# Performance work log

Hardware: AMD Instinct MI355X
Metric: run time of the kernel (lower is better)

## Reference

```python
import jax, jax.numpy as jnp
import numpy as np
from jax import lax

B, K, Z, C, H, W = 32, 7, 64, 3, 64, 64
G = H + 6  # decoder grid for 'small' variant
ITERS = 3
SCALE = Z ** -0.5
EPS = 1e-8


def _pe(h, w):
    # matches SlotAttention.create_positional_embedding: shape [w, h, 4]
    ww = jnp.linspace(0.0, 1.0, w)
    hh = jnp.linspace(0.0, 1.0, h)
    a = jnp.broadcast_to((1.0 - ww)[:, None], (w, h))  # dist_right
    b = jnp.broadcast_to(ww[:, None], (w, h))          # dist_left
    c = jnp.broadcast_to(hh[None, :], (w, h))          # dist_top
    d = jnp.broadcast_to((1.0 - hh)[None, :], (w, h))  # dist_bottom
    return jnp.stack([a, b, c, d], -1)


def _ln(x, g, b):
    m = x.mean(-1, keepdims=True)
    v = ((x - m) ** 2).mean(-1, keepdims=True)
    return (x - m) * lax.rsqrt(v + 1e-5) * g + b


def _conv(x, w, b, p):
    y = lax.conv_general_dilated(x, w, (1, 1), [(p, p), (p, p)],
                                 dimension_numbers=('NCHW', 'OIHW', 'NCHW'))
    return y + b[None, :, None, None]


def setup_inputs() -> dict:
    key = jax.random.key(0)
    ks = iter(jax.random.split(key, 64))
    nrm = lambda shape, s=0.05: jax.random.normal(next(ks), shape, jnp.float32) * s
    d = {}
    d['inputs'] = jax.random.normal(next(ks), (B, C, H, W), jnp.float32)
    d['noise'] = jax.random.normal(next(ks), (B * K, Z), jnp.float32)
    d['enc_pos_w'] = nrm((4, 64)); d['enc_pos_b'] = jnp.zeros(64, jnp.float32)
    d['ec1_w'] = nrm((64, 3, 5, 5)); d['ec1_b'] = jnp.zeros(64, jnp.float32)
    d['ec2_w'] = nrm((64, 64, 5, 5)); d['ec2_b'] = jnp.zeros(64, jnp.float32)
    d['ec3_w'] = nrm((64, 64, 5, 5)); d['ec3_b'] = jnp.zeros(64, jnp.float32)
    d['ec4_w'] = nrm((64, 64, 5, 5)); d['ec4_b'] = jnp.zeros(64, jnp.float32)
    d['ln1_g'] = jnp.ones(64, jnp.float32); d['ln1_b'] = jnp.zeros(64, jnp.float32)
    d['fc1_w'] = nrm((64, 64)); d['fc1_b'] = jnp.zeros(64, jnp.float32)
    d['fc2_w'] = nrm((64, 64)); d['fc2_b'] = jnp.zeros(64, jnp.float32)
    d['lns_g'] = jnp.ones(Z, jnp.float32); d['lns_b'] = jnp.zeros(Z, jnp.float32)
    d['lnf_g'] = jnp.ones(Z, jnp.float32); d['lnf_b'] = jnp.zeros(Z, jnp.float32)
    d['q_w'] = nrm((Z, Z)); d['k_w'] = nrm((64, Z)); d['v_w'] = nrm((64, Z))
    d['mlp1_w'] = nrm((Z, 128)); d['mlp1_b'] = jnp.zeros(128, jnp.float32)
    d['mlp2_w'] = nrm((128, Z)); d['mlp2_b'] = jnp.zeros(Z, jnp.float32)
    d['gru_wih'] = nrm((3 * Z, Z)); d['gru_whh'] = nrm((3 * Z, Z))
    d['gru_bih'] = jnp.zeros(3 * Z, jnp.float32); d['gru_bhh'] = jnp.zeros(3 * Z, jnp.float32)
    d['init_slots'] = jnp.concatenate([jnp.zeros((1, Z), jnp.float32), jnp.ones((1, Z), jnp.float32)], 1)
    d['dec_pos_w'] = nrm((4, Z)); d['dec_pos_b'] = jnp.zeros(Z, jnp.float32)
    d['dc1_w'] = nrm((32, Z, 5, 5)); d['dc1_b'] = jnp.zeros(32, jnp.float32)
    d['dc2_w'] = nrm((32, 32, 5, 5)); d['dc2_b'] = jnp.zeros(32, jnp.float32)
    d['dc3_w'] = nrm((32, 32, 5, 5)); d['dc3_b'] = jnp.zeros(32, jnp.float32)
    d['dc4_w'] = nrm((4, 32, 3, 3)); d['dc4_b'] = jnp.zeros(4, jnp.float32)
    return d


def _forward(inputs, noise, enc_pos_w, enc_pos_b, ec1_w, ec1_b, ec2_w, ec2_b,
             ec3_w, ec3_b, ec4_w, ec4_b, ln1_g, ln1_b, fc1_w, fc1_b, fc2_w, fc2_b,
             lns_g, lns_b, lnf_g, lnf_b, q_w, k_w, v_w, mlp1_w, mlp1_b, mlp2_w,
             mlp2_b, gru_wih, gru_whh, gru_bih, gru_bhh, init_slots, dec_pos_w,
             dec_pos_b, dc1_w, dc1_b, dc2_w, dc2_b, dc3_w, dc3_b, dc4_w, dc4_b):
    # ---- encoder ----
    h = jax.nn.relu(_conv(inputs, ec1_w, ec1_b, 2))
    h = jax.nn.relu(_conv(h, ec2_w, ec2_b, 2))
    h = jax.nn.relu(_conv(h, ec3_w, ec3_b, 2))
    h = jax.nn.relu(_conv(h, ec4_w, ec4_b, 2))
    h = h.transpose(0, 2, 3, 1)                        # [B,H,W,64]
    pe = _pe(H, W) @ enc_pos_w + enc_pos_b             # [W,H,64] (H==W)
    h = h + pe[None]
    feat = h.reshape(B, H * W, 64)
    feat = _ln(feat, ln1_g, ln1_b)
    feat = jax.nn.relu(feat @ fc1_w + fc1_b) @ fc2_w + fc2_b
    k = feat @ k_w                                     # [B,N,Z]
    v = feat @ v_w
    # ---- slot init: Normal(loc, softplus(sp)).rsample() ----
    loc, sp = jnp.split(init_slots, 2, axis=1)
    slots = (loc + jax.nn.softplus(sp) * noise).reshape(B, K, Z)
    # ---- iterative slot attention ----
    for _ in range(ITERS):
        prev = slots
        q = (_ln(prev, lns_g, lns_b) @ q_w) * SCALE
        dots = jnp.einsum('bid,bjd->bij', q, k)        # [B,K,N]
        attn = jax.nn.softmax(dots, axis=1) + EPS      # normalize over slots
        attn = attn / attn.sum(-1, keepdims=True)      # renormalize over keys
        updates = jnp.einsum('bjd,bij->bid', v, attn)  # [B,K,Z]
        # GRU cell (single step), torch gate order r,z,n
        gi = updates.reshape(-1, Z) @ gru_wih.T + gru_bih
        gh = prev.reshape(-1, Z) @ gru_whh.T + gru_bhh
        ir, iz, inn = jnp.split(gi, 3, -1)
        hr, hz, hn = jnp.split(gh, 3, -1)
        r = jax.nn.sigmoid(ir + hr)
        zg = jax.nn.sigmoid(iz + hz)
        n = jnp.tanh(inn + r * hn)
        slots = ((1.0 - zg) * n + zg * prev.reshape(-1, Z)).reshape(B, K, Z)
        slots = slots + (jax.nn.relu(_ln(slots, lnf_g, lnf_b) @ mlp1_w + mlp1_b) @ mlp2_w + mlp2_b)
    # ---- spatial-broadcast decoder ('small') ----
    flat = slots.reshape(B * K, Z)
    zb = jnp.broadcast_to(flat[:, :, None, None], (B * K, Z, G, G))
    pe_d = (_pe(G, G) @ dec_pos_w + dec_pos_b).transpose(2, 0, 1)  # [Z,G,G]
    zb = zb + pe_d[None]
    o = jax.nn.relu(_conv(zb, dc1_w, dc1_b, 1))        # 70->68
    o = jax.nn.relu(_conv(o, dc2_w, dc2_b, 1))         # 68->66
    o = jax.nn.relu(_conv(o, dc3_w, dc3_b, 1))         # 66->64
    o = _conv(o, dc4_w, dc4_b, 1)                      # 64->64, 4ch
    x_loc = jax.nn.sigmoid(o[:, :3]).reshape(B, K, C, H, W)
    mask_logits = o[:, 3].reshape(B, K, 1, H, W)
    mask_logp = jax.nn.log_softmax(mask_logits, axis=1)
    x_orig = (inputs + 1.0) / 2.0
    recon = (x_loc * jnp.exp(mask_logp)).sum(1)
    mse = ((x_orig - recon) ** 2).sum() / B
    return mse, x_loc, mask_logp, slots


def reference(inputs, noise, enc_pos_w, enc_pos_b, ec1_w, ec1_b, ec2_w, ec2_b,
              ec3_w, ec3_b, ec4_w, ec4_b, ln1_g, ln1_b, fc1_w, fc1_b, fc2_w, fc2_b,
              lns_g, lns_b, lnf_g, lnf_b, q_w, k_w, v_w, mlp1_w, mlp1_b, mlp2_w,
              mlp2_b, gru_wih, gru_whh, gru_bih, gru_bhh, init_slots, dec_pos_w,
              dec_pos_b, dc1_w, dc1_b, dc2_w, dc2_b, dc3_w, dc3_b, dc4_w, dc4_b):
    return _forward(inputs, noise, enc_pos_w, enc_pos_b, ec1_w, ec1_b, ec2_w, ec2_b,
                    ec3_w, ec3_b, ec4_w, ec4_b, ln1_g, ln1_b, fc1_w, fc1_b, fc2_w, fc2_b,
                    lns_g, lns_b, lnf_g, lnf_b, q_w, k_w, v_w, mlp1_w, mlp1_b, mlp2_w,
                    mlp2_b, gru_wih, gru_whh, gru_bih, gru_bhh, init_slots, dec_pos_w,
                    dec_pos_b, dc1_w, dc1_b, dc2_w, dc2_b, dc3_w, dc3_b, dc4_w, dc4_b)
```

## Files before the change

kernel.cpp:

```cpp
#include <hip/hip_runtime.h>
#include <math.h>

typedef short bf16x8 __attribute__((ext_vector_type(8)));
typedef float f32x4 __attribute__((ext_vector_type(4)));

#define WS_B0   0u
#define WS_B1   4194304u
#define WS_K    8388608u
#define WS_V    16777216u
#define WS_ATTN 25165824u
#define WS_PART 26083328u
#define WS_ZP   26312704u
#define WS_SLOT 26327040u
#define WS_ROW  26341376u
#define SCALE_ 0.125f

#define OFF_PEB   0u
#define OFF_WCLS  160000u
#define OFF_S     180000u
#define OFF_ZB    250000u

__device__ __forceinline__ float wave_sum(float v) {
#pragma unroll
    for (int m = 32; m >= 1; m >>= 1) v += __shfl_xor(v, m, 64);
    return v;
}
__device__ __forceinline__ unsigned short f2bf(float f) {
    unsigned u = __float_as_uint(f);
    u = u + 0x7fffu + ((u >> 16) & 1u);
    return (unsigned short)(u >> 16);
}
__device__ __forceinline__ float bf2f(unsigned short h) {
    return __uint_as_float(((unsigned)h) << 16);
}
__device__ __forceinline__ void gl_lds16(const void* src, void* lds_base) {
    __builtin_amdgcn_global_load_lds(
        (const __attribute__((address_space(1))) unsigned int*)src,
        (__attribute__((address_space(3))) unsigned int*)lds_base,
        16, 0, 0);
}

__global__ __launch_bounds__(256) void pack_weights(
    const float* __restrict__ w, unsigned short* __restrict__ wp,
    int CIN, int COUT_STORE, int KS, int NT, int total)
{
    int t = blockIdx.x * 256 + threadIdx.x;
    if (t >= total) return;
    int lane = t & 63;
    int nt = (t >> 6) % NT;
    int ch = t / (64 * NT);
    int CPT = CIN / 32;
    int cic = ch % CPT;
    int tap = ch / CPT;
    int ky = tap / KS, kx = tap % KS;
    int co = nt * 16 + (lane & 15);
    int k0 = cic * 32 + (lane >> 4) * 8;
    unsigned short v[8];
#pragma unroll
    for (int j = 0; j < 8; ++j) {
        int ci = k0 + j;
        float f = (co < COUT_STORE) ? w[((size_t)(co * CIN + ci) * KS + ky) * KS + kx] : 0.f;
        v[j] = f2bf(f);
    }
    *(uint4*)(wp + (size_t)t * 8) = *(uint4*)v;
}

__global__ __launch_bounds__(256) void pack_weights3(
    const float* __restrict__ w0, const float* __restrict__ w1,
    const float* __restrict__ w2, unsigned short* __restrict__ wp,
    float* __restrict__ zpage)
{
    if (blockIdx.x == 0 && threadIdx.x < 64) zpage[threadIdx.x] = 0.f;
    int t = blockIdx.x * 256 + threadIdx.x;
    if (t >= 38400) return;
    int which = t / 12800;
    int tt = t % 12800;
    const float* w = (which == 0) ? w0 : ((which == 1) ? w1 : w2);
    unsigned short* dst = wp + (size_t)which * 102400;
    int lane = tt & 63;
    int nt = (tt >> 6) & 3;
    int ch = tt >> 8;
    int cic = ch & 1;
    int tap = ch >> 1;
    int ky = tap / 5, kx = tap % 5;
    int co = nt * 16 + (lane & 15);
    int k0 = cic * 32 + (lane >> 4) * 8;
    unsigned short v[8];
#pragma unroll
    for (int j = 0; j < 8; ++j) {
        int ci = k0 + j;
        v[j] = f2bf(w[((size_t)(co * 64 + ci) * 5 + ky) * 5 + kx]);
    }
    *(uint4*)(dst + (size_t)tt * 8) = *(uint4*)v;
}

__global__ __launch_bounds__(256) void pack_fc4(
    const float* __restrict__ w0, const float* __restrict__ w1,
    const float* __restrict__ w2, const float* __restrict__ w3,
    unsigned short* __restrict__ wp)
{
    int t = blockIdx.x * 256 + threadIdx.x;
    if (t >= 2048) return;
    int which = t / 512;
    int tt = t % 512;
    const float* w = (which == 0) ? w0 : ((which == 1) ? w1 : ((which == 2) ? w2 : w3));
    unsigned short* dst = wp + (size_t)which * 4096;
    int lane = tt & 63;
    int nt = (tt >> 6) & 3;
    int ck = tt >> 8;
    int n = nt * 16 + (lane & 15);
    int k0 = ck * 32 + (lane >> 4) * 8;
    unsigned short v[8];
#pragma unroll
    for (int j = 0; j < 8; ++j) v[j] = f2bf(w[(size_t)(k0 + j) * 64 + n]);
    *(uint4*)(dst + (size_t)tt * 8) = *(uint4*)v;
}

template<int CIN, int NTT, int NTU, int KS, int PAD, int NSTORE, int RELU, int OUTF32>
__global__ __launch_bounds__(256) void conv_mfma(
    const unsigned short* __restrict__ in, const unsigned short* __restrict__ wpack,
    const float* __restrict__ bias, void* __restrict__ outv,
    const unsigned short* __restrict__ zpage,
    int Hin, int Win, int Hout, int Wout, int tilesX, int tilesY)
{
    constexpr int TS = 16, TH = TS + KS - 1;
    constexpr int CPT = CIN / 32;
    constexpr int G8 = CIN / 8;
    constexpr int CS = NTT / NTU;
    constexpr int TOTCH = TH * TH * G8;
    constexpr int TOTCH_PAD = (TOTCH + 63) & ~63;
    __shared__ __align__(16) unsigned short tile[TOTCH_PAD * 8];
    const int tpb = tilesX * tilesY;
    const int blk = blockIdx.x;
    const int n = blk / (tpb * CS);
    const int rem = blk % (tpb * CS);
    const int t = rem / CS;
    const int cog = rem % CS;
    const int ntb = cog * NTU;
    const int ty0 = (t / tilesX) * TS, tx0 = (t % tilesX) * TS;
    const int tid = threadIdx.x;
    const int wv = tid >> 6, lane = tid & 63;

    const unsigned short* inb = in + (size_t)n * Hin * Win * CIN;
    for (int cb = wv * 64; cb < TOTCH; cb += 256) {
        const int idx = cb + lane;
        const int r = idx / (TH * G8);
        const int p = idx % (TH * G8);
        const int c = p / G8;
        const int chunk = p % G8;
        const int g = (chunk - c) & (G8 - 1);
        const int iy = ty0 - PAD + r, ix = tx0 - PAD + c;
        const bool ok = (idx < TOTCH) && ((unsigned)iy < (unsigned)Hin) && ((unsigned)ix < (unsigned)Win);
        const unsigned short* src = ok ? (inb + ((size_t)iy * Win + ix) * CIN + g * 8) : zpage;
        gl_lds16(src, tile + (size_t)cb * 8);
    }
    __syncthreads();

    const int q = lane >> 4, m = lane & 15;
    const int row0 = wv * 4;
    f32x4 acc[4][NTU];
#pragma unroll
    for (int mt = 0; mt < 4; ++mt)
#pragma unroll
        for (int nt = 0; nt < NTU; ++nt) acc[mt][nt] = (f32x4){0.f, 0.f, 0.f, 0.f};

#pragma unroll
    for (int cic = 0; cic < CPT; ++cic) {
#pragma unroll
        for (int kx = 0; kx < KS; ++kx) {
            bf16x8 B[KS][NTU];
#pragma unroll
            for (int ky = 0; ky < KS; ++ky)
#pragma unroll
                for (int nt = 0; nt < NTU; ++nt)
                    B[ky][nt] = *(const bf16x8*)(wpack +
                        ((size_t)(((ky * KS + kx) * CPT + cic) * NTT + ntb + nt) * 64 + lane) * 8);
            const int cbase = m + kx;
            const int slot = (cic * 32 + q * 8 + cbase * 8) % CIN;
#pragma unroll
            for (int ir = 0; ir < KS + 3; ++ir) {
                bf16x8 afr = *(const bf16x8*)&tile[((row0 + ir) * TH + cbase) * CIN + slot];
#pragma unroll
                for (int ky = 0; ky < KS; ++ky) {
                    const int mt = ir - ky;
                    if (mt < 0 || mt > 3) continue;
#pragma unroll
                    for (int nt = 0; nt < NTU; ++nt)
                        acc[mt][nt] = __builtin_amdgcn_mfma_f32_16x16x32_bf16(afr, B[ky][nt], acc[mt][nt], 0, 0, 0);
                }
            }
        }
    }

#pragma unroll
    for (int nt = 0; nt < NTU; ++nt) {
        const int co = (ntb + nt) * 16 + m;
        const float bv = (co < NSTORE) ? bias[co] : 0.f;
#pragma unroll
        for (int mt = 0; mt < 4; ++mt) {
            const int oy = ty0 + wv * 4 + mt;
#pragma unroll
            for (int j = 0; j < 4; ++j) {
                const int ox = tx0 + q * 4 + j;
                if (oy < Hout && ox < Wout && co < NSTORE) {
                    float v = acc[mt][nt][j] + bv;
                    if (RELU) v = fmaxf(v, 0.f);
                    size_t o = (((size_t)n * Hout + oy) * Wout + ox) * NSTORE + co;
                    if (OUTF32) ((float*)outv)[o] = v;
                    else ((unsigned short*)outv)[o] = f2bf(v);
                }
            }
        }
    }
}

__global__ __launch_bounds__(256) void pe_synth(
    const float* __restrict__ dpw, const float* __restrict__ dpb,
    unsigned short* __restrict__ peb, float* __restrict__ zbias)
{
    const int tid = threadIdx.x;
    if (blockIdx.x == 0 && tid < 32) zbias[tid] = 0.f;
    const int pix = blockIdx.x * 256 + tid;
    if (pix >= 4900) return;
    const int iy = pix / 70, ix = pix % 70;
    const float fy = iy * (1.f / 69.f), fx = ix * (1.f / 69.f);
    unsigned short v[64];
#pragma unroll
    for (int ci = 0; ci < 64; ++ci) {
        float p = (1.f - fy) * dpw[ci] + fy * dpw[64 + ci]
                + fx * dpw[128 + ci] + (1.f - fx) * dpw[192 + ci] + dpb[ci];
        v[ci] = f2bf(p);
    }
    uint4* ob = (uint4*)(peb + (size_t)pix * 64);
#pragma unroll
    for (int i = 0; i < 8; ++i) ob[i] = ((uint4*)v)[i];
}

__global__ __launch_bounds__(256) void wcls_build(
    const float* __restrict__ w, float* __restrict__ wcls)
{
    int idx = blockIdx.x * 256 + threadIdx.x;
    if (idx >= 9 * 32 * 64) return;
    int cls = idx / (32 * 64);
    int co = (idx / 64) % 32;
    int ci = idx % 64;
    int rc = cls / 3, cc = cls % 3;
    int ky0 = (rc == 0) ? 1 : 0, ky1 = (rc == 2) ? 3 : 4;
    int kx0 = (cc == 0) ? 1 : 0, kx1 = (cc == 2) ? 3 : 4;
    float s = 0.f;
    const float* wb = w + (size_t)(co * 64 + ci) * 25;
    for (int ky = ky0; ky <= ky1; ++ky)
        for (int kx = kx0; kx <= kx1; ++kx)
            s += wb[ky * 5 + kx];
    wcls[idx] = s;
}

__global__ __launch_bounds__(256) void slot_s(
    const float* __restrict__ slots, const float* __restrict__ wcls,
    float* __restrict__ S)
{
    int idx = blockIdx.x * 256 + threadIdx.x;
    if (idx >= 224 * 9 * 32) return;
    int n = idx / (9 * 32);
    int cls = (idx / 32) % 9;
    int co = idx % 32;
    const float* sl = slots + n * 64;
    const float* wc = wcls + (size_t)(cls * 32 + co) * 64;
    float s = 0.f;
#pragma unroll
    for (int ci = 0; ci < 64; ++ci) s = fmaf(sl[ci], wc[ci], s);
    S[idx] = s;
}

__global__ __launch_bounds__(256) void dc1_assemble(
    const float* __restrict__ P, const float* __restrict__ S,
    const float* __restrict__ bias, int n0,
    unsigned short* __restrict__ out)
{
    const int gid = blockIdx.x * 256 + threadIdx.x;
    const int nl = gid / 4624;
    const int pix = gid % 4624;
    const int oy = pix / 68, ox = pix % 68;
    const int rc = (oy == 0) ? 0 : ((oy == 67) ? 2 : 1);
    const int cc = (ox == 0) ? 0 : ((ox == 67) ? 2 : 1);
    const float* Sp = S + ((size_t)(n0 + nl) * 9 + (rc * 3 + cc)) * 32;
    const float* Pp = P + (size_t)pix * 32;
    unsigned short v[32];
#pragma unroll
    for (int co = 0; co < 32; ++co)
        v[co] = f2bf(fmaxf(bias[co] + Pp[co] + Sp[co], 0.f));
    uint4* ob = (uint4*)(out + ((size_t)nl * 4624 + pix) * 32);
#pragma unroll
    for (int i = 0; i < 4; ++i) ob[i] = ((uint4*)v)[i];
}

__global__ __launch_bounds__(256) void conv_ec1(
    const float* __restrict__ in, const float* __restrict__ wts,
    const float* __restrict__ bias, unsigned short* __restrict__ out)
{
    __shared__ float tile[3][20][21];
    const int blk = blockIdx.x;
    const int n = blk >> 6;
    const int sub = blk & 63;
    const int t = sub >> 2;
    const int cog = sub & 3;
    const int ty0 = (t >> 2) * 16, tx0 = (t & 3) * 16;
    const int tid = threadIdx.x;
    for (int idx = tid; idx < 1200; idx += 256) {
        int ci = idx / 400, rc = idx % 400;
        int r = rc / 20, c = rc % 20;
        int gy = ty0 + r - 2, gx = tx0 + c - 2;
        float v = 0.f;
        if (gy >= 0 && gy < 64 && gx >= 0 && gx < 64)
            v = in[((size_t)n * 3 + ci) * 4096 + gy * 64 + gx];
        tile[ci][r][c] = v;
    }
    __syncthreads();
    const int lx = tid & 15, ly = tid >> 4;
    float acc[16];
#pragma unroll
    for (int co = 0; co < 16; ++co) acc[co] = bias[cog * 16 + co];
    for (int ci = 0; ci < 3; ++ci) {
        float val[25];
#pragma unroll
        for (int ky = 0; ky < 5; ++ky)
#pragma unroll
            for (int kx = 0; kx < 5; ++kx) val[ky * 5 + kx] = tile[ci][ly + ky][lx + kx];
#pragma unroll
        for (int co = 0; co < 16; ++co) {
            const float* wc = wts + (size_t)((cog * 16 + co) * 3 + ci) * 25;
            float a = acc[co];
#pragma unroll
            for (int tt = 0; tt < 25; ++tt) a = fmaf(val[tt], wc[tt], a);
            acc[co] = a;
        }
    }
    unsigned short tmp[16];
#pragma unroll
    for (int co = 0; co < 16; ++co) tmp[co] = f2bf(fmaxf(acc[co], 0.f));
    uint4* ob = (uint4*)(out + (((size_t)n * 64 + ty0 + ly) * 64 + tx0 + lx) * 64 + cog * 16);
    ob[0] = ((uint4*)tmp)[0];
    ob[1] = ((uint4*)tmp)[1];
}

__global__ __launch_bounds__(256) void encoder_tail_mfma(
    const unsigned short* __restrict__ h4,
    const float* __restrict__ epw, const float* __restrict__ epb,
    const float* __restrict__ ln1g, const float* __restrict__ ln1b,
    const unsigned short* __restrict__ pfc1, const float* __restrict__ fc1b,
    const unsigned short* __restrict__ pfc2, const float* __restrict__ fc2b,
    const unsigned short* __restrict__ pkw, const unsigned short* __restrict__ pvw,
    unsigned short* __restrict__ kout, unsigned short* __restrict__ vout)
{
    __shared__ __align__(16) unsigned short X[64][72];
    const int b = blockIdx.x >> 6;
    const int y = blockIdx.x & 63;
    const int tid = threadIdx.x;

    {
        const int p = tid >> 2, sub = tid & 3;
        const unsigned short* hp = h4 + ((((size_t)b * 64 + y) * 64 + p) * 64) + sub * 16;
        unsigned short raw[16];
        *(uint4*)(raw)     = *(const uint4*)hp;
        *(uint4*)(raw + 8) = *(const uint4*)(hp + 8);
        const float fy = y * (1.f / 63.f), fx = p * (1.f / 63.f);
        float f[16];
        float s1 = 0.f, s2 = 0.f;
#pragma unroll
        for (int j = 0; j < 16; ++j) {
            int ch = sub * 16 + j;
            float pe = (1.f - fy) * epw[ch] + fy * epw[64 + ch]
                     + fx * epw[128 + ch] + (1.f - fx) * epw[192 + ch] + epb[ch];
            float v = bf2f(raw[j]) + pe;
            f[j] = v;
            s1 += v;
            s2 += v * v;
        }
        s1 += __shfl_xor(s1, 1, 64); s1 += __shfl_xor(s1, 2, 64);
        s2 += __shfl_xor(s2, 1, 64); s2 += __shfl_xor(s2, 2, 64);
        const float m = s1 * (1.f / 64.f);
        const float var = s2 * (1.f / 64.f) - m * m;
        const float inv = rsqrtf(var + 1e-5f);
        unsigned short xb[16];
#pragma unroll
        for (int j = 0; j < 16; ++j) {
            int ch = sub * 16 + j;
            xb[j] = f2bf((f[j] - m) * inv * ln1g[ch] + ln1b[ch]);
        }
        *(uint4*)&X[p][sub * 16]     = ((uint4*)xb)[0];
        *(uint4*)&X[p][sub * 16 + 8] = ((uint4*)xb)[1];
    }
    __syncthreads();

    const int w = tid >> 6, lane = tid & 63;
    const int q = lane >> 4, m_ = lane & 15;
    const int row0 = w * 16;

    {
        f32x4 a1[4];
#pragma unroll
        for (int nt = 0; nt < 4; ++nt) a1[nt] = (f32x4){0.f, 0.f, 0.f, 0.f};
#pragma unroll
        for (int ck = 0; ck < 2; ++ck) {
            bf16x8 afr = *(const bf16x8*)&X[row0 + m_][ck * 32 + q * 8];
#pragma unroll
            for (int nt = 0; nt < 4; ++nt) {
                bf16x8 bfr = *(const bf16x8*)(pfc1 + ((size_t)((ck * 4 + nt) * 64 + lane)) * 8);
                a1[nt] = __builtin_amdgcn_mfma_f32_16x16x32_bf16(afr, bfr, a1[nt], 0, 0, 0);
            }
        }
        __syncthreads();
#pragma unroll
        for (int nt = 0; nt < 4; ++nt) {
            const float bb = fc1b[nt * 16 + m_];
#pragma unroll
            for (int reg = 0; reg < 4; ++reg)
                X[row0 + q * 4 + reg][nt * 16 + m_] = f2bf(fmaxf(a1[nt][reg] + bb, 0.f));
        }
    }
    __syncthreads();

    {
        f32x4 a2[4];
#pragma unroll
        for (int nt = 0; nt < 4; ++nt) a2[nt] = (f32x4){0.f, 0.f, 0.f, 0.f};
#pragma unroll
        for (int ck = 0; ck < 2; ++ck) {
            bf16x8 afr = *(const bf16x8*)&X[row0 + m_][ck * 32 + q * 8];
#pragma unroll
            for (int nt = 0; nt < 4; ++nt) {
                bf16x8 bfr = *(const bf16x8*)(pfc2 + ((size_t)((ck * 4 + nt) * 64 + lane)) * 8);
                a2[nt] = __builtin_amdgcn_mfma_f32_16x16x32_bf16(afr, bfr, a2[nt], 0, 0, 0);
            }
        }
        __syncthreads();
#pragma unroll
        for (int nt = 0; nt < 4; ++nt) {
            const float bb = fc2b[nt * 16 + m_];
#pragma unroll
            for (int reg = 0; reg < 4; ++reg)
                X[row0 + q * 4 + reg][nt * 16 + m_] = f2bf(a2[nt][reg] + bb);
        }
    }
    __syncthreads();

    {
        f32x4 ak[4], av[4];
#pragma unroll
        for (int nt = 0; nt < 4; ++nt) {
            ak[nt] = (f32x4){0.f, 0.f, 0.f, 0.f};
            av[nt] = (f32x4){0.f, 0.f, 0.f, 0.f};
        }
#pragma unroll
        for (int ck = 0; ck < 2; ++ck) {
            bf16x8 afr = *(const bf16x8*)&X[row0 + m_][ck * 32 + q * 8];
#pragma unroll
            for (int nt = 0; nt < 4; ++nt) {
                bf16x8 bk = *(const bf16x8*)(pkw + ((size_t)((ck * 4 + nt) * 64 + lane)) * 8);
                bf16x8 bv = *(const bf16x8*)(pvw + ((size_t)((ck * 4 + nt) * 64 + lane)) * 8);
                ak[nt] = __builtin_amdgcn_mfma_f32_16x16x32_bf16(afr, bk, ak[nt], 0, 0, 0);
                av[nt] = __builtin_amdgcn_mfma_f32_16x16x32_bf16(afr, bv, av[nt], 0, 0, 0);
            }
        }
        const size_t base = ((size_t)b * 4096) + y * 64 + row0;
#pragma unroll
        for (int nt = 0; nt < 4; ++nt) {
            const int ch = nt * 16 + m_;
#pragma unroll
            for (int reg = 0; reg < 4; ++reg) {
                const size_t o = (base + q * 4 + reg) * 64 + ch;
                kout[o] = f2bf(ak[nt][reg]);
                vout[o] = f2bf(av[nt][reg]);
            }
        }
    }
}

__global__ __launch_bounds__(256) void slot_init(
    const float* __restrict__ noise, const float* __restrict__ init_slots,
    float* __restrict__ slots, float* __restrict__ rowsum)
{
    int i = blockIdx.x * 256 + threadIdx.x;
    if (i < 224) rowsum[i] = 0.f;
    if (i < 224 * 64) {
        int z = i & 63;
        float spl = log1pf(expf(init_slots[64 + z]));
        slots[i] = init_slots[z] + spl * noise[i];
    }
}

__global__ __launch_bounds__(256) void attn_fused(
    const unsigned short* __restrict__ kbuf, const unsigned short* __restrict__ vbuf,
    const float* __restrict__ slots,
    const float* __restrict__ lnsg, const float* __restrict__ lnsb,
    const float* __restrict__ qw,
    float* __restrict__ part, float* __restrict__ rowsum)
{
    __shared__ float qs[7][64];
    __shared__ float ash[256][7];
    __shared__ float red7[7][4];
    __shared__ float redv[4][7][64];
    const int b = blockIdx.x >> 4;
    const int js = blockIdx.x & 15;
    const int j0 = js * 256;
    const int tid = threadIdx.x;
    const int lane = tid & 63, wv = tid >> 6;

    for (int i = wv; i < 7; i += 4) {
        float s = slots[(b * 7 + i) * 64 + lane];
        float m = wave_sum(s) * (1.f / 64.f);
        float d = s - m;
        float var = wave_sum(d * d) * (1.f / 64.f);
        float x = d * rsqrtf(var + 1e-5f) * lnsg[lane] + lnsb[lane];
        float qv = 0.f;
        for (int c = 0; c < 64; ++c) qv = fmaf(__shfl(x, c, 64), qw[c * 64 + lane], qv);
        qs[i][lane] = qv * SCALE_;
    }
    __syncthreads();

    {
        const int j = j0 + tid;
        float kr[64];
        const unsigned short* kp = kbuf + (((size_t)b * 4096) + j) * 64;
#pragma unroll
        for (int d8 = 0; d8 < 8; ++d8) {
            uint4 kv = ((const uint4*)kp)[d8];
            const unsigned short* h = (const unsigned short*)&kv;
#pragma unroll
            for (int z = 0; z < 8; ++z) kr[d8 * 8 + z] = bf2f(h[z]);
        }
        float dots[7];
#pragma unroll
        for (int i = 0; i < 7; ++i) {
            float a = 0.f;
#pragma unroll
            for (int d = 0; d < 64; ++d) a = fmaf(kr[d], qs[i][d], a);
            dots[i] = a;
        }
        float mx = dots[0];
#pragma unroll
        for (int i = 1; i < 7; ++i) mx = fmaxf(mx, dots[i]);
        float sum = 0.f;
#pragma unroll
        for (int i = 0; i < 7; ++i) { dots[i] = expf(dots[i] - mx); sum += dots[i]; }
        const float inv = 1.f / sum;
#pragma unroll
        for (int i = 0; i < 7; ++i) {
            float a = dots[i] * inv + 1e-8f;
            dots[i] = a;
            ash[tid][i] = a;
        }
#pragma unroll
        for (int i = 0; i < 7; ++i) {
            float s = wave_sum(dots[i]);
            if (lane == 0) red7[i][wv] = s;
        }
    }
    __syncthreads();
    if (tid < 7)
        atomicAdd(&rowsum[b * 7 + tid], red7[tid][0] + red7[tid][1] + red7[tid][2] + red7[tid][3]);

    {
        const int d = lane, jc = wv;
        float acc[7];
#pragma unroll
        for (int i = 0; i < 7; ++i) acc[i] = 0.f;
        for (int jl = jc; jl < 256; jl += 4) {
            float av = bf2f(vbuf[(((size_t)b * 4096) + j0 + jl) * 64 + d]);
#pragma unroll
            for (int i = 0; i < 7; ++i)
                acc[i] = fmaf(ash[jl][i], av, acc[i]);
        }
#pragma unroll
        for (int i = 0; i < 7; ++i) redv[jc][i][d] = acc[i];
    }
    __syncthreads();
    if (tid < 7 * 64) {
        int i = tid / 64, dd = tid % 64;
        float s = redv[0][i][dd] + redv[1][i][dd] + redv[2][i][dd] + redv[3][i][dd];
        part[((((size_t)b * 16) + js) * 7 + i) * 64 + dd] = s;
    }
}

__global__ __launch_bounds__(64) void gru_mlp(
    float* __restrict__ slots, const float* __restrict__ part,
    float* __restrict__ rowsum,
    const float* __restrict__ wih, const float* __restrict__ whh,
    const float* __restrict__ bih, const float* __restrict__ bhh,
    const float* __restrict__ lnfg, const float* __restrict__ lnfb,
    const float* __restrict__ m1w, const float* __restrict__ m1b,
    const float* __restrict__ m2w, const float* __restrict__ m2b)
{
    const int n = blockIdx.x;
    const int b = n / 7, i = n % 7;
    const int l = threadIdx.x;
    float upd = 0.f;
    for (int js = 0; js < 16; ++js)
        upd += part[((((size_t)b * 16) + js) * 7 + i) * 64 + l];
    upd /= rowsum[n];
    if (l == 0) rowsum[n] = 0.f;
    const float prev = slots[n * 64 + l];
    float gi0 = bih[l], gi1 = bih[64 + l], gi2 = bih[128 + l];
    float gh0 = bhh[l], gh1 = bhh[64 + l], gh2 = bhh[128 + l];
    for (int c = 0; c < 64; ++c) {
        float u = __shfl(upd, c, 64), p = __shfl(prev, c, 64);
        gi0 = fmaf(u, wih[l * 64 + c], gi0);
        gi1 = fmaf(u, wih[(64 + l) * 64 + c], gi1);
        gi2 = fmaf(u, wih[(128 + l) * 64 + c], gi2);
        gh0 = fmaf(p, whh[l * 64 + c], gh0);
        gh1 = fmaf(p, whh[(64 + l) * 64 + c], gh1);
        gh2 = fmaf(p, whh[(128 + l) * 64 + c], gh2);
    }
    float r  = 1.f / (1.f + expf(-(gi0 + gh0)));
    float zg = 1.f / (1.f + expf(-(gi1 + gh1)));
    float nn = tanhf(gi2 + r * gh2);
    float s = (1.f - zg) * nn + zg * prev;
    float m = wave_sum(s) * (1.f / 64.f);
    float d = s - m;
    float var = wave_sum(d * d) * (1.f / 64.f);
    float x = d * rsqrtf(var + 1e-5f) * lnfg[l] + lnfb[l];
    float h0 = m1b[l], h1 = m1b[64 + l];
    for (int c = 0; c < 64; ++c) {
        float xv = __shfl(x, c, 64);
        h0 = fmaf(xv, m1w[c * 128 + l], h0);
        h1 = fmaf(xv, m1w[c * 128 + 64 + l], h1);
    }
    h0 = fmaxf(h0, 0.f); h1 = fmaxf(h1, 0.f);
    float o = m2b[l];
    for (int c = 0; c < 64; ++c) {
        o = fmaf(__shfl(h0, c, 64), m2w[c * 64 + l], o);
        o = fmaf(__shfl(h1, c, 64), m2w[(64 + c) * 64 + l], o);
    }
    slots[n * 64 + l] = s + o;
}

__global__ __launch_bounds__(256) void finalize_k(
    const float* __restrict__ dc4out, const float* __restrict__ inputs,
    float* __restrict__ out)
{
    const int tid = threadIdx.x;
    const int gp = blockIdx.x * 256 + tid;
    const int b = gp >> 12, p = gp & 4095;
    float4 o4[7];
#pragma unroll
    for (int k = 0; k < 7; ++k)
        o4[k] = ((const float4*)dc4out)[(size_t)(b * 7 + k) * 4096 + p];
    float mx = o4[0].w;
#pragma unroll
    for (int k = 1; k < 7; ++k) mx = fmaxf(mx, o4[k].w);
    float s = 0.f;
#pragma unroll
    for (int k = 0; k < 7; ++k) s += expf(o4[k].w - mx);
    const float lse = mx + logf(s);
    float recon0 = 0.f, recon1 = 0.f, recon2 = 0.f;
    float* xl = out + 1;
    float* ml = out + 2752513;
#pragma unroll
    for (int k = 0; k < 7; ++k) {
        float lp = o4[k].w - lse;
        ml[((size_t)(b * 7 + k)) * 4096 + p] = lp;
        float w = expf(lp);
        float x0 = 1.f / (1.f + expf(-o4[k].x));
        float x1 = 1.f / (1.f + expf(-o4[k].y));
        float x2 = 1.f / (1.f + expf(-o4[k].z));
        xl[(((size_t)(b * 7 + k)) * 3 + 0) * 4096 + p] = x0;
        xl[(((size_t)(b * 7 + k)) * 3 + 1) * 4096 + p] = x1;
        xl[(((size_t)(b * 7 + k)) * 3 + 2) * 4096 + p] = x2;
        recon0 = fmaf(x0, w, recon0);
        recon1 = fmaf(x1, w, recon1);
        recon2 = fmaf(x2, w, recon2);
    }
    float err = 0.f;
    {
        float xo = (inputs[((size_t)b * 3 + 0) * 4096 + p] + 1.f) * 0.5f;
        float dd = xo - recon0; err += dd * dd;
        xo = (inputs[((size_t)b * 3 + 1) * 4096 + p] + 1.f) * 0.5f;
        dd = xo - recon1; err += dd * dd;
        xo = (inputs[((size_t)b * 3 + 2) * 4096 + p] + 1.f) * 0.5f;
        dd = xo - recon2; err += dd * dd;
    }
    float wsum = wave_sum(err);
    __shared__ float red[4];
    const int lane = tid & 63, wv = tid >> 6;
    if (lane == 0) red[wv] = wsum;
    __syncthreads();
    if (tid == 0) atomicAdd(out, (red[0] + red[1] + red[2] + red[3]) * (1.f / 32.f));
}

__global__ __launch_bounds__(256) void copy_slots(const float* __restrict__ slots,
                                                  float* __restrict__ out)
{
    int i = blockIdx.x * 256 + threadIdx.x;
    if (i == 0) out[0] = 0.f;
    if (i < 14336) out[3670017 + i] = slots[i];
}

extern "C" void kernel_launch(void* const* d_in, const int* in_sizes, int n_in,
                              void* d_out, int out_size, void* d_ws, size_t ws_size,
                              hipStream_t stream) {
    (void)in_sizes; (void)n_in; (void)out_size; (void)ws_size;
    const float* inputs = (const float*)d_in[0];
    const float* noise  = (const float*)d_in[1];
    const float* epw  = (const float*)d_in[2];
    const float* epb  = (const float*)d_in[3];
    const float* ec1w = (const float*)d_in[4];
    const float* ec1b = (const float*)d_in[5];
    const float* ec2w = (const float*)d_in[6];
    const float* ec2b = (const float*)d_in[7];
    const float* ec3w = (const float*)d_in[8];
    const float* ec3b = (const float*)d_in[9];
    const float* ec4w = (const float*)d_in[10];
    const float* ec4b = (const float*)d_in[11];
    const float* ln1g = (const float*)d_in[12];
    const float* ln1b = (const float*)d_in[13];
    const float* fc1w = (const float*)d_in[14];
    const float* fc1b = (const float*)d_in[15];
    const float* fc2w = (const float*)d_in[16];
    const float* fc2b = (const float*)d_in[17];
    const float* lnsg = (const float*)d_in[18];
    const float* lnsb = (const float*)d_in[19];
    const float* lnfg = (const float*)d_in[20];
    const float* lnfb = (const float*)d_in[21];
    const float* qw   = (const float*)d_in[22];
    const float* kw   = (const float*)d_in[23];
    const float* vw   = (const float*)d_in[24];
    const float* m1w  = (const float*)d_in[25];
    const float* m1b  = (const float*)d_in[26];
    const float* m2w  = (const float*)d_in[27];
    const float* m2b  = (const float*)d_in[28];
    const float* wih  = (const float*)d_in[29];
    const float* whh  = (const float*)d_in[30];
    const float* bih  = (const float*)d_in[31];
    const float* bhh  = (const float*)d_in[32];
    const float* init_slots = (const float*)d_in[33];
    const float* dpw  = (const float*)d_in[34];
    const float* dpb  = (const float*)d_in[35];
    const float* dc1w = (const float*)d_in[36];
    const float* dc1b = (const float*)d_in[37];
    const float* dc2w = (const float*)d_in[38];
    const float* dc2b = (const float*)d_in[39];
    const float* dc3w = (const float*)d_in[40];
    const float* dc3b = (const float*)d_in[41];
    const float* dc4w = (const float*)d_in[42];
    const float* dc4b = (const float*)d_in[43];

    float* ws = (float*)d_ws;
    unsigned short* B0 = (unsigned short*)(ws + WS_B0);
    unsigned short* B1 = (unsigned short*)(ws + WS_B1);
    unsigned short* K = (unsigned short*)(ws + WS_K);
    unsigned short* V = (unsigned short*)(ws + WS_V);
    unsigned short* dping = (unsigned short*)(ws + WS_B0);
    unsigned short* dpong = (unsigned short*)(ws + WS_K);
    float* dc4out = ws + WS_V;
    unsigned short* PK = (unsigned short*)(ws + WS_V + 4194304u);
    unsigned short* p_ec2 = PK, *p_ec3 = PK + 102400, *p_ec4 = PK + 204800;
    unsigned short* p_dc1 = PK, *p_dc2 = PK + 51200, *p_dc3 = PK + 76800, *p_dc4 = PK + 102400;
    float* attn  = ws + WS_ATTN;
    unsigned short* PFC = (unsigned short*)attn;
    unsigned short* p_fc1 = PFC, *p_fc2 = PFC + 4096, *p_kw = PFC + 8192, *p_vw = PFC + 12288;
    unsigned short* peb = (unsigned short*)(attn + OFF_PEB);
    float* wclsb = attn + OFF_WCLS;
    float* Sbuf  = attn + OFF_S;
    float* zbias = attn + OFF_ZB;
    float* part  = ws + WS_PART;
    float* P     = ws + WS_PART;
    float* zpage = ws + WS_ZP;
    float* slots = ws + WS_SLOT;
    float* rowsum = ws + WS_ROW;
    float* out = (float*)d_out;
    const unsigned short* zp16 = (const unsigned short*)zpage;

    pack_weights3<<<150, 256, 0, stream>>>(ec2w, ec3w, ec4w, p_ec2, zpage);
    pack_fc4<<<8, 256, 0, stream>>>(fc1w, fc2w, kw, vw, p_fc1);

    conv_ec1<<<2048, 256, 0, stream>>>(inputs, ec1w, ec1b, B0);
    conv_mfma<64, 4, 4, 5, 2, 64, 1, 0><<<512, 256, 0, stream>>>(B0, p_ec2, ec2b, B1, zp16, 64, 64, 64, 64, 4, 4);
    conv_mfma<64, 4, 4, 5, 2, 64, 1, 0><<<512, 256, 0, stream>>>(B1, p_ec3, ec3b, B0, zp16, 64, 64, 64, 64, 4, 4);
    conv_mfma<64, 4, 4, 5, 2, 64, 1, 0><<<512, 256, 0, stream>>>(B0, p_ec4, ec4b, B1, zp16, 64, 64, 64, 64, 4, 4);
    encoder_tail_mfma<<<2048, 256, 0, stream>>>(B1, epw, epb, ln1g, ln1b,
                                                p_fc1, fc1b, p_fc2, fc2b, p_kw, p_vw, K, V);
    slot_init<<<56, 256, 0, stream>>>(noise, init_slots, slots, rowsum);

    for (int it = 0; it < 3; ++it) {
        attn_fused<<<512, 256, 0, stream>>>(K, V, slots, lnsg, lnsb, qw, part, rowsum);
        gru_mlp<<<224, 64, 0, stream>>>(slots, part, rowsum, wih, whh, bih, bhh,
                                        lnfg, lnfb, m1w, m1b, m2w, m2b);
    }

    pack_weights<<<25, 256, 0, stream>>>(dc1w, p_dc1, 64, 32, 5, 2, 6400);
    pack_weights<<<13, 256, 0, stream>>>(dc2w, p_dc2, 32, 32, 5, 2, 3200);
    pack_weights<<<13, 256, 0, stream>>>(dc3w, p_dc3, 32, 32, 5, 2, 3200);
    pack_weights<<<3, 256, 0, stream>>>(dc4w, p_dc4, 32, 4, 3, 1, 576);
    pe_synth<<<20, 256, 0, stream>>>(dpw, dpb, peb, zbias);
    conv_mfma<64, 2, 2, 5, 1, 32, 0, 1><<<25, 256, 0, stream>>>(peb, p_dc1, zbias, P, zp16, 70, 70, 68, 68, 5, 5);
    wcls_build<<<72, 256, 0, stream>>>(dc1w, wclsb);
    slot_s<<<252, 256, 0, stream>>>(slots, wclsb, Sbuf);

    for (int ch = 0; ch < 2; ++ch) {
        float* d4o = dc4out + (size_t)ch * 112 * 4 * 4096;
        dc1_assemble<<<2023, 256, 0, stream>>>(P, Sbuf, dc1b, ch * 112, dping);
        conv_mfma<32, 2, 2, 5, 1, 32, 1, 0><<<2800, 256, 0, stream>>>(dping, p_dc2, dc2b, dpong, zp16, 68, 68, 66, 66, 5, 5);
        conv_mfma<32, 2, 2, 5, 1, 32, 1, 0><<<1792, 256, 0, stream>>>(dpong, p_dc3, dc3b, dping, zp16, 66, 66, 64, 64, 4, 4);
        conv_mfma<32, 1, 1, 3, 1, 4, 0, 1><<<1792, 256, 0, stream>>>(dping, p_dc4, dc4b, d4o, zp16, 64, 64, 64, 64, 4, 4);
    }

    copy_slots<<<56, 256, 0, stream>>>(slots, out);
    finalize_k<<<512, 256, 0, stream>>>(dc4out, inputs, out);
}
```

Measured before the change: 741.0 us.

## Merge small prep kernels into fused launches and split encoder conv channels

```diff
diff --git a/kernel.cpp b/kernel.cpp
--- a/kernel.cpp
+++ b/kernel.cpp
@@ -16,7 +16,6 @@
 #define SCALE_ 0.125f
 
 #define OFF_PEB   0u
-#define OFF_WCLS  160000u
 #define OFF_S     180000u
 #define OFF_ZB    250000u
 
@@ -40,12 +39,10 @@
         16, 0, 0);
 }
 
-__global__ __launch_bounds__(256) void pack_weights(
+__device__ __forceinline__ void pack_one(
     const float* __restrict__ w, unsigned short* __restrict__ wp,
-    int CIN, int COUT_STORE, int KS, int NT, int total)
-{
-    int t = blockIdx.x * 256 + threadIdx.x;
-    if (t >= total) return;
+    int CIN, int COUT_STORE, int KS, int NT, int t)
+{
     int lane = t & 63;
     int nt = (t >> 6) % NT;
     int ch = t / (64 * NT);
@@ -65,55 +62,100 @@
     *(uint4*)(wp + (size_t)t * 8) = *(uint4*)v;
 }
 
-__global__ __launch_bounds__(256) void pack_weights3(
-    const float* __restrict__ w0, const float* __restrict__ w1,
-    const float* __restrict__ w2, unsigned short* __restrict__ wp,
-    float* __restrict__ zpage)
+__global__ __launch_bounds__(256) void pack_enc(
+    const float* __restrict__ ec2w, const float* __restrict__ ec3w,
+    const float* __restrict__ ec4w, unsigned short* __restrict__ wp,
+    const float* __restrict__ fc1w, const float* __restrict__ fc2w,
+    const float* __restrict__ kw, const float* __restrict__ vw,
+    unsigned short* __restrict__ pfc, float* __restrict__ zpage)
 {
     if (blockIdx.x == 0 && threadIdx.x < 64) zpage[threadIdx.x] = 0.f;
     int t = blockIdx.x * 256 + threadIdx.x;
-    if (t >= 38400) return;
-    int which = t / 12800;
-    int tt = t % 12800;
-    const float* w = (which == 0) ? w0 : ((which == 1) ? w1 : w2);
-    unsigned short* dst = wp + (size_t)which * 102400;
-    int lane = tt & 63;
-    int nt = (tt >> 6) & 3;
-    int ch = tt >> 8;
-    int cic = ch & 1;
-    int tap = ch >> 1;
-    int ky = tap / 5, kx = tap % 5;
-    int co = nt * 16 + (lane & 15);
-    int k0 = cic * 32 + (lane >> 4) * 8;
-    unsigned short v[8];
-#pragma unroll
-    for (int j = 0; j < 8; ++j) {
-        int ci = k0 + j;
-        v[j] = f2bf(w[((size_t)(co * 64 + ci) * 5 + ky) * 5 + kx]);
-    }
-    *(uint4*)(dst + (size_t)tt * 8) = *(uint4*)v;
-}
-
-__global__ __launch_bounds__(256) void pack_fc4(
-    const float* __restrict__ w0, const float* __restrict__ w1,
-    const float* __restrict__ w2, const float* __restrict__ w3,
-    unsigned short* __restrict__ wp)
+    if (t < 38400) {
+        int which = t / 12800;
+        int tt = t % 12800;
+        const float* w = (which == 0) ? ec2w : ((which == 1) ? ec3w : ec4w);
+        pack_one(w, wp + (size_t)which * 102400, 64, 64, 5, 4, tt);
+        return;
+    }
+    t -= 38400;
+    if (t < 2048) {
+        int which = t / 512;
+        int tt = t % 512;
+        const float* w = (which == 0) ? fc1w : ((which == 1) ? fc2w : ((which == 2) ? kw : vw));
+        unsigned short* dst = pfc + (size_t)which * 4096;
+        int lane = tt & 63;
+        int nt = (tt >> 6) & 3;
+        int ck = tt >> 8;
+        int n = nt * 16 + (lane & 15);
+        int k0 = ck * 32 + (lane >> 4) * 8;
+        unsigned short v[8];
+#pragma unroll
+        for (int j = 0; j < 8; ++j) v[j] = f2bf(w[(size_t)(k0 + j) * 64 + n]);
+        *(uint4*)(dst + (size_t)tt * 8) = *(uint4*)v;
+    }
+}
+
+__global__ __launch_bounds__(256) void dec_prep(
+    const float* __restrict__ dc1w, const float* __restrict__ dc2w,
+    const float* __restrict__ dc3w, const float* __restrict__ dc4w,
+    unsigned short* __restrict__ p_dc1, unsigned short* __restrict__ p_dc2,
+    unsigned short* __restrict__ p_dc3, unsigned short* __restrict__ p_dc4,
+    const float* __restrict__ dpw, const float* __restrict__ dpb,
+    unsigned short* __restrict__ peb, float* __restrict__ zbias,
+    const float* __restrict__ slots, float* __restrict__ S,
+    float* __restrict__ out)
 {
     int t = blockIdx.x * 256 + threadIdx.x;
-    if (t >= 2048) return;
-    int which = t / 512;
-    int tt = t % 512;
-    const float* w = (which == 0) ? w0 : ((which == 1) ? w1 : ((which == 2) ? w2 : w3));
-    unsigned short* dst = wp + (size_t)which * 4096;
-    int lane = tt & 63;
-    int nt = (tt >> 6) & 3;
-    int ck = tt >> 8;
-    int n = nt * 16 + (lane & 15);
-    int k0 = ck * 32 + (lane >> 4) * 8;
-    unsigned short v[8];
-#pragma unroll
-    for (int j = 0; j < 8; ++j) v[j] = f2bf(w[(size_t)(k0 + j) * 64 + n]);
-    *(uint4*)(dst + (size_t)tt * 8) = *(uint4*)v;
+    if (t < 6400) { pack_one(dc1w, p_dc1, 64, 32, 5, 2, t); return; }
+    t -= 6400;
+    if (t < 3200) { pack_one(dc2w, p_dc2, 32, 32, 5, 2, t); return; }
+    t -= 3200;
+    if (t < 3200) { pack_one(dc3w, p_dc3, 32, 32, 5, 2, t); return; }
+    t -= 3200;
+    if (t < 576)  { pack_one(dc4w, p_dc4, 32, 4, 3, 1, t); return; }
+    t -= 576;
+    if (t < 4900) {
+        const int iy = t / 70, ix = t % 70;
+        const float fy = iy * (1.f / 69.f), fx = ix * (1.f / 69.f);
+        unsigned short v[64];
+#pragma unroll
+        for (int ci = 0; ci < 64; ++ci) {
+            float p = (1.f - fy) * dpw[ci] + fy * dpw[64 + ci]
+                    + fx * dpw[128 + ci] + (1.f - fx) * dpw[192 + ci] + dpb[ci];
+            v[ci] = f2bf(p);
+        }
+        uint4* ob = (uint4*)(peb + (size_t)t * 64);
+#pragma unroll
+        for (int i = 0; i < 8; ++i) ob[i] = ((uint4*)v)[i];
+        return;
+    }
+    t -= 4900;
+    if (t < 224 * 9 * 32) {
+        int n = t / (9 * 32);
+        int cls = (t / 32) % 9;
+        int co = t % 32;
+        int rc = cls / 3, cc = cls % 3;
+        int ky0 = (rc == 0) ? 1 : 0, ky1 = (rc == 2) ? 3 : 4;
+        int kx0 = (cc == 0) ? 1 : 0, kx1 = (cc == 2) ? 3 : 4;
+        const float* sl = slots + n * 64;
+        float s = 0.f;
+        for (int ci = 0; ci < 64; ++ci) {
+            const float* wb = dc1w + (size_t)(co * 64 + ci) * 25;
+            float wsum = 0.f;
+            for (int ky = ky0; ky <= ky1; ++ky)
+                for (int kx = kx0; kx <= kx1; ++kx)
+                    wsum += wb[ky * 5 + kx];
+            s = fmaf(sl[ci], wsum, s);
+        }
+        S[t] = s;
+        return;
+    }
+    t -= 224 * 9 * 32;
+    if (t < 14336) { out[3670017 + t] = slots[t]; return; }
+    t -= 14336;
+    if (t < 32) zbias[t] = 0.f;
+    else if (t == 32) out[0] = 0.f;
 }
 
 template<int CIN, int NTT, int NTU, int KS, int PAD, int NSTORE, int RELU, int OUTF32>
@@ -212,64 +254,6 @@
             }
         }
     }
-}
-
-__global__ __launch_bounds__(256) void pe_synth(
-    const float* __restrict__ dpw, const float* __restrict__ dpb,
-    unsigned short* __restrict__ peb, float* __restrict__ zbias)
-{
-    const int tid = threadIdx.x;
-    if (blockIdx.x == 0 && tid < 32) zbias[tid] = 0.f;
-    const int pix = blockIdx.x * 256 + tid;
-    if (pix >= 4900) return;
-    const int iy = pix / 70, ix = pix % 70;
-    const float fy = iy * (1.f / 69.f), fx = ix * (1.f / 69.f);
-    unsigned short v[64];
-#pragma unroll
-    for (int ci = 0; ci < 64; ++ci) {
-        float p = (1.f - fy) * dpw[ci] + fy * dpw[64 + ci]
-                + fx * dpw[128 + ci] + (1.f - fx) * dpw[192 + ci] + dpb[ci];
-        v[ci] = f2bf(p);
-    }
-    uint4* ob = (uint4*)(peb + (size_t)pix * 64);
-#pragma unroll
-    for (int i = 0; i < 8; ++i) ob[i] = ((uint4*)v)[i];
-}
-
-__global__ __launch_bounds__(256) void wcls_build(
-    const float* __restrict__ w, float* __restrict__ wcls)
-{
-    int idx = blockIdx.x * 256 + threadIdx.x;
-    if (idx >= 9 * 32 * 64) return;
-    int cls = idx / (32 * 64);
-    int co = (idx / 64) % 32;
-    int ci = idx % 64;
-    int rc = cls / 3, cc = cls % 3;
-    int ky0 = (rc == 0) ? 1 : 0, ky1 = (rc == 2) ? 3 : 4;
-    int kx0 = (cc == 0) ? 1 : 0, kx1 = (cc == 2) ? 3 : 4;
-    float s = 0.f;
-    const float* wb = w + (size_t)(co * 64 + ci) * 25;
-    for (int ky = ky0; ky <= ky1; ++ky)
-        for (int kx = kx0; kx <= kx1; ++kx)
-            s += wb[ky * 5 + kx];
-    wcls[idx] = s;
-}
-
-__global__ __launch_bounds__(256) void slot_s(
-    const float* __restrict__ slots, const float* __restrict__ wcls,
-    float* __restrict__ S)
-{
-    int idx = blockIdx.x * 256 + threadIdx.x;
-    if (idx >= 224 * 9 * 32) return;
-    int n = idx / (9 * 32);
-    int cls = (idx / 32) % 9;
-    int co = idx % 32;
-    const float* sl = slots + n * 64;
-    const float* wc = wcls + (size_t)(cls * 32 + co) * 64;
-    float s = 0.f;
-#pragma unroll
-    for (int ci = 0; ci < 64; ++ci) s = fmaf(sl[ci], wc[ci], s);
-    S[idx] = s;
 }
 
 __global__ __launch_bounds__(256) void dc1_assemble(
@@ -685,14 +669,6 @@
     if (lane == 0) red[wv] = wsum;
     __syncthreads();
     if (tid == 0) atomicAdd(out, (red[0] + red[1] + red[2] + red[3]) * (1.f / 32.f));
-}
-
-__global__ __launch_bounds__(256) void copy_slots(const float* __restrict__ slots,
-                                                  float* __restrict__ out)
-{
-    int i = blockIdx.x * 256 + threadIdx.x;
-    if (i == 0) out[0] = 0.f;
-    if (i < 14336) out[3670017 + i] = slots[i];
 }
 
 extern "C" void kernel_launch(void* const* d_in, const int* in_sizes, int n_in,
@@ -757,9 +733,8 @@
     unsigned short* p_dc1 = PK, *p_dc2 = PK + 51200, *p_dc3 = PK + 76800, *p_dc4 = PK + 102400;
     float* attn  = ws + WS_ATTN;
     unsigned short* PFC = (unsigned short*)attn;
-    unsigned short* p_fc1 = PFC, *p_fc2 = PFC + 4096, *p_kw = PFC + 8192, *p_vw = PFC + 12288;
+    unsigned short* p_fc1 = PFC;
     unsigned short* peb = (unsigned short*)(attn + OFF_PEB);
-    float* wclsb = attn + OFF_WCLS;
     float* Sbuf  = attn + OFF_S;
     float* zbias = attn + OFF_ZB;
     float* part  = ws + WS_PART;
@@ -770,15 +745,16 @@
     float* out = (float*)d_out;
     const unsigned short* zp16 = (const unsigned short*)zpage;
 
-    pack_weights3<<<150, 256, 0, stream>>>(ec2w, ec3w, ec4w, p_ec2, zpage);
-    pack_fc4<<<8, 256, 0, stream>>>(fc1w, fc2w, kw, vw, p_fc1);
+    pack_enc<<<159, 256, 0, stream>>>(ec2w, ec3w, ec4w, p_ec2,
+                                      fc1w, fc2w, kw, vw, p_fc1, zpage);
 
     conv_ec1<<<2048, 256, 0, stream>>>(inputs, ec1w, ec1b, B0);
-    conv_mfma<64, 4, 4, 5, 2, 64, 1, 0><<<512, 256, 0, stream>>>(B0, p_ec2, ec2b, B1, zp16, 64, 64, 64, 64, 4, 4);
-    conv_mfma<64, 4, 4, 5, 2, 64, 1, 0><<<512, 256, 0, stream>>>(B1, p_ec3, ec3b, B0, zp16, 64, 64, 64, 64, 4, 4);
-    conv_mfma<64, 4, 4, 5, 2, 64, 1, 0><<<512, 256, 0, stream>>>(B0, p_ec4, ec4b, B1, zp16, 64, 64, 64, 64, 4, 4);
+    conv_mfma<64, 4, 2, 5, 2, 64, 1, 0><<<1024, 256, 0, stream>>>(B0, p_ec2, ec2b, B1, zp16, 64, 64, 64, 64, 4, 4);
+    conv_mfma<64, 4, 2, 5, 2, 64, 1, 0><<<1024, 256, 0, stream>>>(B1, p_ec3, ec3b, B0, zp16, 64, 64, 64, 64, 4, 4);
+    conv_mfma<64, 4, 2, 5, 2, 64, 1, 0><<<1024, 256, 0, stream>>>(B0, p_ec4, ec4b, B1, zp16, 64, 64, 64, 64, 4, 4);
     encoder_tail_mfma<<<2048, 256, 0, stream>>>(B1, epw, epb, ln1g, ln1b,
-                                                p_fc1, fc1b, p_fc2, fc2b, p_kw, p_vw, K, V);
+                                                p_fc1, fc1b, p_fc1 + 4096, fc2b,
+                                                p_fc1 + 8192, p_fc1 + 12288, K, V);
     slot_init<<<56, 256, 0, stream>>>(noise, init_slots, slots, rowsum);
 
     for (int it = 0; it < 3; ++it) {
@@ -787,14 +763,10 @@
                                         lnfg, lnfb, m1w, m1b, m2w, m2b);
     }
 
-    pack_weights<<<25, 256, 0, stream>>>(dc1w, p_dc1, 64, 32, 5, 2, 6400);
-    pack_weights<<<13, 256, 0, stream>>>(dc2w, p_dc2, 32, 32, 5, 2, 3200);
-    pack_weights<<<13, 256, 0, stream>>>(dc3w, p_dc3, 32, 32, 5, 2, 3200);
-    pack_weights<<<3, 256, 0, stream>>>(dc4w, p_dc4, 32, 4, 3, 1, 576);
-    pe_synth<<<20, 256, 0, stream>>>(dpw, dpb, peb, zbias);
+    dec_prep<<<380, 256, 0, stream>>>(dc1w, dc2w, dc3w, dc4w,
+                                      p_dc1, p_dc2, p_dc3, p_dc4,
+                                      dpw, dpb, peb, zbias, slots, Sbuf, out);
     conv_mfma<64, 2, 2, 5, 1, 32, 0, 1><<<25, 256, 0, stream>>>(peb, p_dc1, zbias, P, zp16, 70, 70, 68, 68, 5, 5);
-    wcls_build<<<72, 256, 0, stream>>>(dc1w, wclsb);
-    slot_s<<<252, 256, 0, stream>>>(slots, wclsb, Sbuf);
 
     for (int ch = 0; ch < 2; ++ch) {
         float* d4o = dc4out + (size_t)ch * 112 * 4 * 4096;
@@ -804,6 +776,5 @@
         conv_mfma<32, 1, 1, 3, 1, 4, 0, 1><<<1792, 256, 0, stream>>>(dping, p_dc4, dc4b, d4o, zp16, 64, 64, 64, 64, 4, 4);
     }
 
-    copy_slots<<<56, 256, 0, stream>>>(slots, out);
     finalize_k<<<512, 256, 0, stream>>>(dc4out, inputs, out);
 }
```

Measured after the change: 847.1 us. +14.3%, slower.
